# Optimization experiments

Measured on AMD Instinct MI355X. Metric: run time of the kernel, lower is better.

Reference implementation:

```python
import jax, jax.numpy as jnp
import numpy as np

EMBED_DIM = 1024
NUM_HEADS = 16
MICRO_HEADS = 8
HEAD_DIM = EMBED_DIM // NUM_HEADS
N_BLOCKS = NUM_HEADS // MICRO_HEADS
B, N = 2, 2048


def setup_inputs() -> dict:
    key = jax.random.key(0)
    ks = jax.random.split(key, 9)
    s = 1.0 / np.sqrt(EMBED_DIM)
    return {
        "x": jax.random.normal(ks[0], (B, N, EMBED_DIM), dtype=jnp.float32),
        "Wq": jax.random.uniform(ks[1], (EMBED_DIM, EMBED_DIM), jnp.float32, -s, s),
        "bq": jax.random.uniform(ks[2], (EMBED_DIM,), jnp.float32, -s, s),
        "Wk": jax.random.uniform(ks[3], (EMBED_DIM, EMBED_DIM), jnp.float32, -s, s),
        "bk": jax.random.uniform(ks[4], (EMBED_DIM,), jnp.float32, -s, s),
        "Wv": jax.random.uniform(ks[5], (EMBED_DIM, EMBED_DIM), jnp.float32, -s, s),
        "bv": jax.random.uniform(ks[6], (EMBED_DIM,), jnp.float32, -s, s),
        "Wo": jax.random.uniform(ks[7], (EMBED_DIM, EMBED_DIM), jnp.float32, -s, s),
        "bo": jax.random.uniform(ks[8], (EMBED_DIM,), jnp.float32, -s, s),
    }


def _scramble(t, b, n):
    # Replicates torch's Qh[:, :, hs:he, :].contiguous().view(B*mh, N, dh)
    # which is a raw row-major reshape mixing (N, mh) -> (mh, N) per batch.
    # (B, N, E) -> (B, N, nb, mh, dh) -> (B, nb, N, mh, dh) -> raw reshape -> (B, nb, mh, N, dh)
    t = t.reshape(b, n, N_BLOCKS, MICRO_HEADS, HEAD_DIM)
    t = jnp.transpose(t, (0, 2, 1, 3, 4))
    return t.reshape(b, N_BLOCKS, MICRO_HEADS, n, HEAD_DIM)


def reference(x, Wq, bq, Wk, bk, Wv, bv, Wo, bo):
    b, n, e = x.shape
    scale = HEAD_DIM ** -0.5
    Q = x @ Wq.T + bq
    K = x @ Wk.T + bk
    V = x @ Wv.T + bv
    q = _scramble(Q, b, n)  # (B, nb, mh, N, dh)
    k = _scramble(K, b, n)
    v = _scramble(V, b, n)
    s = jnp.einsum("bgmqd,bgmkd->bgmqk", q, k) * scale  # (B, nb, mh, N, N)
    causal = jnp.tril(jnp.ones((n, n), dtype=bool))
    s = jnp.where(causal, s, -jnp.inf)
    p = jax.nn.softmax(s, axis=-1)
    ctx = jnp.einsum("bgmqk,bgmkd->bgmqd", p, v)  # (B, nb, mh, N, dh)
    # inverse raw reshape: (mh, N, dh) -> (N, mh*dh) per (b, g), then concat blocks
    ctx = ctx.reshape(b, N_BLOCKS, n, MICRO_HEADS * HEAD_DIM)
    ctx = jnp.transpose(ctx, (0, 2, 1, 3)).reshape(b, n, e)
    return ctx @ Wo.T + bo
```

## Files before the change

### kernel.cpp

```cpp
#include <hip/hip_runtime.h>
#include <hip/hip_bf16.h>


typedef unsigned short ushortT;
typedef __attribute__((ext_vector_type(8))) short short8;
typedef __attribute__((ext_vector_type(4))) float floatx4;

__device__ inline float bf2f(ushortT u) {
    union { unsigned int i; float f; } v; v.i = ((unsigned int)u) << 16; return v.f;
}
__device__ inline ushortT f2bf(float f) {
    union { float f; unsigned int i; } v; v.f = f;
    unsigned int x = v.i;
    return (ushortT)((x + 0x7fffu + ((x >> 16) & 1u)) >> 16);
}

__device__ inline void gl_lds16(const ushortT* g, ushortT* lds) {
    __builtin_amdgcn_global_load_lds(
        (const __attribute__((address_space(1))) unsigned int*)g,
        (__attribute__((address_space(3))) unsigned int*)lds, 16, 0, 0);
}

__global__ __launch_bounds__(256) void cvt_bf16(
    const float* __restrict__ x,
    const float* __restrict__ Wq, const float* __restrict__ Wk,
    const float* __restrict__ Wv, const float* __restrict__ Wo,
    ushortT* __restrict__ xb, ushortT* __restrict__ Wb)
{
    const unsigned tid = blockIdx.x * 256 + threadIdx.x;
    const size_t e = (size_t)tid * 8;
    const float* src;
    ushortT* dst;
    size_t off;
    if (e < (size_t)(4u << 20)) { src = x; dst = xb; off = e; }
    else {
        const size_t r = e - (size_t)(4u << 20);
        const int wsel = (int)(r >> 20);
        off = r & 0xFFFFFu;
        src = (wsel == 0) ? Wq : (wsel == 1) ? Wk : (wsel == 2) ? Wv : Wo;
        dst = Wb + ((size_t)wsel << 20);
    }
    const float4 f0 = ((const float4*)(src + off))[0];
    const float4 f1 = ((const float4*)(src + off))[1];
    union { __hip_bfloat162 h[4]; uint4 u; } pk;
    pk.h[0] = __float22bfloat162_rn(float2{f0.x, f0.y});
    pk.h[1] = __float22bfloat162_rn(float2{f0.z, f0.w});
    pk.h[2] = __float22bfloat162_rn(float2{f1.x, f1.y});
    pk.h[3] = __float22bfloat162_rn(float2{f1.z, f1.w});
    *(uint4*)(dst + off) = pk.u;
}

template <bool OUT_F32>
__global__ __launch_bounds__(256) void gemm_lds(
    const ushortT* __restrict__ A, const ushortT* __restrict__ Wst,
    const float* __restrict__ b0, const float* __restrict__ b1, const float* __restrict__ b2,
    void* __restrict__ O0, void* __restrict__ O1, void* __restrict__ O2)
{
    __shared__ __align__(16) ushortT As[128 * 64];
    __shared__ __align__(16) ushortT Bs[128 * 64];
    const int t = threadIdx.x;
    const int m0 = blockIdx.y * 128;
    const int n0g = blockIdx.x * 128;
    const int mat = n0g >> 10;
    const int n0 = n0g & 1023;
    const ushortT* W = Wst + ((size_t)mat << 20);
    const float* bias = (mat == 0) ? b0 : (mat == 1) ? b1 : b2;
    void* Out        = (mat == 0) ? O0 : (mat == 1) ? O1 : O2;

    const int w = t >> 6, lane = t & 63;
    const int wm = w >> 1, wn = w & 1;
    const int col16 = lane & 15, quad = lane >> 4;

    floatx4 acc[4][4];
    for (int i = 0; i < 4; i++)
        for (int j = 0; j < 4; j++) acc[i][j] = (floatx4)0.0f;

    const int cid0 = w * 256 + lane;

    for (int k0 = 0; k0 < 1024; k0 += 64) {
        #pragma unroll
        for (int q = 0; q < 4; q++) {
            const int cid = cid0 + q * 64;
            const int row = cid >> 3;
            const int sch = (cid & 7) ^ (row & 7);
            ushortT* dstA = As + (size_t)(w * 256 + q * 64) * 8;
            ushortT* dstB = Bs + (size_t)(w * 256 + q * 64) * 8;
            gl_lds16(A + (size_t)(m0 + row) * 1024 + k0 + sch * 8, dstA);
            gl_lds16(W + (size_t)(n0 + row) * 1024 + k0 + sch * 8, dstB);
        }
        __syncthreads();
        #pragma unroll
        for (int ks = 0; ks < 64; ks += 32) {
            const int cbase = (ks >> 3) + quad;
            const int sw = col16 & 7;
            short8 a[4], b[4];
            #pragma unroll
            for (int i = 0; i < 4; i++) {
                const int row = wm * 64 + i * 16 + col16;
                a[i] = *(const short8*)(As + row * 64 + ((cbase ^ sw) << 3));
            }
            #pragma unroll
            for (int j = 0; j < 4; j++) {
                const int row = wn * 64 + j * 16 + col16;
                b[j] = *(const short8*)(Bs + row * 64 + ((cbase ^ sw) << 3));
            }
            #pragma unroll
            for (int i = 0; i < 4; i++)
                #pragma unroll
                for (int j = 0; j < 4; j++)
                    acc[i][j] = __builtin_amdgcn_mfma_f32_16x16x32_bf16(a[i], b[j], acc[i][j], 0, 0, 0);
        }
        __syncthreads();
    }

    for (int j = 0; j < 4; j++) {
        const int colg = n0 + wn * 64 + j * 16 + col16;
        const float bv = bias[colg];
        for (int i = 0; i < 4; i++) {
            const int rbase = m0 + wm * 64 + i * 16 + quad * 4;
            for (int r = 0; r < 4; r++) {
                const float val = acc[i][j][r] + bv;
                if constexpr (OUT_F32)
                    ((float*)Out)[(size_t)(rbase + r) * 1024 + colg] = val;
                else
                    ((ushortT*)Out)[(size_t)(rbase + r) * 1024 + colg] = f2bf(val);
            }
        }
    }
}

__global__ __launch_bounds__(256) void transpose_v(
    const ushortT* __restrict__ Vb, ushortT* __restrict__ VT)
{
    __shared__ ushortT L[64 * 65];
    const int bid = blockIdx.x;
    const int pt = bid & 31, s = bid >> 5;
    const int bb = s >> 4, g = (s >> 3) & 1, mh = s & 7;
    const size_t baseoff = (size_t)bb * 2048 * 1024 + (size_t)g * 512;
    const int t = threadIdx.x;
    {
        const int pr = t >> 2, seg = t & 3;
        const int i = mh * 2048 + pt * 64 + pr;
        const uint4* src = (const uint4*)(Vb + baseoff + (size_t)(i >> 3) * 1024 + (i & 7) * 64 + seg * 16);
        union { uint4 u[2]; ushortT h[16]; } tmp;
        tmp.u[0] = src[0]; tmp.u[1] = src[1];
        #pragma unroll
        for (int d = 0; d < 16; d++) L[pr * 65 + seg * 16 + d] = tmp.h[d];
    }
    __syncthreads();
    {
        const int dc = t >> 2, pseg = t & 3;
        union { uint4 u[2]; ushortT h[16]; } tmp;
        #pragma unroll
        for (int j = 0; j < 16; j++) tmp.h[j] = L[(pseg * 16 + j) * 65 + dc];
        uint4* dst = (uint4*)(VT + (size_t)s * 64 * 2048 + (size_t)dc * 2048 + pt * 64 + pseg * 16);
        dst[0] = tmp.u[0]; dst[1] = tmp.u[1];
    }
}

__global__ __launch_bounds__(256) void attn(
    const ushortT* __restrict__ Qb, const ushortT* __restrict__ Kb,
    const ushortT* __restrict__ VT, ushortT* __restrict__ Cb)
{
    __shared__ __align__(16) ushortT Qs[128 * 72];
    __shared__ __align__(16) ushortT Ks[2][64 * 64];
    __shared__ __align__(16) ushortT Vs[2][64 * 64];
    __shared__ __align__(16) ushortT Ps[64 * 72];

    const int t = threadIdx.x;
    const int bid = blockIdx.x;
    const int xcd = bid & 7;
    const int jj  = bid >> 3;
    const int s   = xcd * 4 + (jj >> 4);
    const int p   = jj & 15;
    const int qtA = p, qtB = 31 - p;
    const int bb = s >> 4, g = (s >> 3) & 1, mh = s & 7;

    const int w = t >> 6, lane = t & 63;
    const int col16 = lane & 15, quad = lane >> 4;

    const size_t baseoff = (size_t)bb * 2048 * 1024 + (size_t)g * 512;
    const size_t vtbase  = (size_t)s * 64 * 2048;
    const int i0A = mh * 2048 + qtA * 64;
    const int i0B = mh * 2048 + qtB * 64;
    const int qloc = w * 16 + col16;
    const float KL = 0.125f * 1.44269504f;

    {
        const int row = t >> 1, half = t & 1;
        const int i = ((row < 64) ? i0A : i0B) + (row & 63);
        const uint4* src = (const uint4*)(Qb + baseoff + (size_t)(i >> 3) * 1024 + (i & 7) * 64 + half * 32);
        uint4* dst = (uint4*)(Qs + row * 72 + half * 32);
        dst[0] = src[0]; dst[1] = src[1]; dst[2] = src[2]; dst[3] = src[3];
    }

    auto stageKV = [&](int kt, int bsel) {
        ushortT* kd = &Ks[bsel][0] + (size_t)(w * 128) * 8;
        ushortT* vd = &Vs[bsel][0] + (size_t)(w * 128) * 8;
        #pragma unroll
        for (int q = 0; q < 2; q++) {
            const int cid = w * 128 + q * 64 + lane;
            const int row = cid >> 3;
            const int sch = (cid & 7) ^ (row & 7);
            const int jr = mh * 2048 + kt * 64 + row;
            gl_lds16(Kb + baseoff + (size_t)(jr >> 3) * 1024 + (jr & 7) * 64 + sch * 8,
                     kd + q * 64 * 8);
            gl_lds16(VT + vtbase + (size_t)row * 2048 + kt * 64 + sch * 8,
                     vd + q * 64 * 8);
        }
    };

    float m_s[2] = {-1e30f, -1e30f};
    float l_s[2] = {0.f, 0.f};
    floatx4 Oacc[2][4];
    for (int tl = 0; tl < 2; tl++)
        for (int c = 0; c < 4; c++) Oacc[tl][c] = (floatx4)0.0f;

    stageKV(0, 0);
    const int ktmax = qtB;
    for (int kt = 0; kt <= ktmax; ++kt) {
        const int bsel = kt & 1;
        __syncthreads();
        if (kt < ktmax) stageKV(kt + 1, bsel ^ 1);

        #pragma unroll
        for (int tile = 0; tile < 2; ++tile) {
            const int qt = tile ? qtB : qtA;
            if (kt > qt) continue;
            const int qsrow = (tile ? 64 : 0) + qloc;

            floatx4 sc[4];
            for (int c = 0; c < 4; c++) sc[c] = (floatx4)0.0f;
            #pragma unroll
            for (int ks = 0; ks < 64; ks += 32) {
                const short8 bq = *(const short8*)(Qs + qsrow * 72 + ks + quad * 8);
                #pragma unroll
                for (int c = 0; c < 4; c++) {
                    const int krow = c * 16 + col16;
                    const short8 ak = *(const short8*)(&Ks[bsel][0] + krow * 64 +
                                        ((((ks >> 3) + quad) ^ (krow & 7)) << 3));
                    sc[c] = __builtin_amdgcn_mfma_f32_16x16x32_bf16(ak, bq, sc[c], 0, 0, 0);
                }
            }

            const bool diag = (kt == qt);
            float mx = -1e30f;
            #pragma unroll
            for (int c = 0; c < 4; c++)
                #pragma unroll
                for (int r = 0; r < 4; r++) {
                    float v = sc[c][r];
                    if (diag && (c * 16 + quad * 4 + r) > qloc) v = -1e30f;
                    sc[c][r] = v;
                    mx = fmaxf(mx, v);
                }
            mx = fmaxf(mx, __shfl_xor(mx, 16));
            mx = fmaxf(mx, __shfl_xor(mx, 32));
            const float mold = m_s[tile];
            const float mnew = fmaxf(mold, mx);
            const float alpha = exp2f((mold - mnew) * KL);
            m_s[tile] = mnew;
            float sum = 0.f;
            #pragma unroll
            for (int c = 0; c < 4; c++)
                #pragma unroll
                for (int r = 0; r < 4; r++) {
                    const float pv = exp2f((sc[c][r] - mnew) * KL);
                    sc[c][r] = pv;
                    sum += pv;
                }
            sum += __shfl_xor(sum, 16);
            sum += __shfl_xor(sum, 32);
            l_s[tile] = l_s[tile] * alpha + sum;
            #pragma unroll
            for (int c = 0; c < 4; c++) Oacc[tile][c] *= alpha;

            #pragma unroll
            for (int c = 0; c < 4; c++)
                #pragma unroll
                for (int rp = 0; rp < 2; rp++) {
                    union { ushortT h[2]; unsigned int u; } pk;
                    pk.h[0] = f2bf(sc[c][rp * 2]);
                    pk.h[1] = f2bf(sc[c][rp * 2 + 1]);
                    *(unsigned int*)(Ps + qloc * 72 + c * 16 + quad * 4 + rp * 2) = pk.u;
                }

            #pragma unroll
            for (int kk = 0; kk < 64; kk += 32) {
                const short8 bp = *(const short8*)(Ps + qloc * 72 + kk + quad * 8);
                #pragma unroll
                for (int c = 0; c < 4; c++) {
                    const int drow = c * 16 + col16;
                    const short8 av = *(const short8*)(&Vs[bsel][0] + drow * 64 +
                                        ((((kk >> 3) + quad) ^ (drow & 7)) << 3));
                    Oacc[tile][c] = __builtin_amdgcn_mfma_f32_16x16x32_bf16(av, bp, Oacc[tile][c], 0, 0, 0);
                }
            }
        }
    }

    #pragma unroll
    for (int tile = 0; tile < 2; ++tile) {
        const int i = (tile ? i0B : i0A) + qloc;
        const float inv = 1.0f / l_s[tile];
        ushortT* dst = Cb + baseoff + (size_t)(i >> 3) * 1024 + (i & 7) * 64;
        #pragma unroll
        for (int c = 0; c < 4; c++)
            #pragma unroll
            for (int rp = 0; rp < 2; rp++) {
                union { ushortT h[2]; unsigned int u; } pk;
                pk.h[0] = f2bf(Oacc[tile][c][rp * 2] * inv);
                pk.h[1] = f2bf(Oacc[tile][c][rp * 2 + 1] * inv);
                *(unsigned int*)(dst + c * 16 + quad * 4 + rp * 2) = pk.u;
            }
    }
}

extern "C" void kernel_launch(void* const* d_in, const int* in_sizes, int n_in,
                              void* d_out, int out_size, void* d_ws, size_t ws_size,
                              hipStream_t stream)
{
    const float* x  = (const float*)d_in[0];
    const float* Wq = (const float*)d_in[1];
    const float* bq = (const float*)d_in[2];
    const float* Wk = (const float*)d_in[3];
    const float* bk = (const float*)d_in[4];
    const float* Wv = (const float*)d_in[5];
    const float* bv = (const float*)d_in[6];
    const float* Wo = (const float*)d_in[7];
    const float* bo = (const float*)d_in[8];

    const size_t M1 = (size_t)1024 * 1024;
    ushortT* Wb  = (ushortT*)d_ws;
    ushortT* xb  = Wb + 4 * M1;
    ushortT* Qb  = xb + 4 * M1;
    ushortT* Kb  = Qb + 4 * M1;
    ushortT* Vb  = (ushortT*)d_out;
    ushortT* VTb = xb;
    ushortT* Cb  = Qb;

    dim3 blk(256);
    cvt_bf16<<<dim3(4096), blk, 0, stream>>>(x, Wq, Wk, Wv, Wo, xb, Wb);
    gemm_lds<false><<<dim3(24, 32), blk, 0, stream>>>(
        xb, Wb, bq, bk, bv, Qb, Kb, Vb);
    transpose_v<<<dim3(1024), blk, 0, stream>>>(Vb, VTb);
    attn<<<dim3(512), blk, 0, stream>>>(Qb, Kb, VTb, Cb);
    gemm_lds<true><<<dim3(8, 32), blk, 0, stream>>>(
        Cb, Wb + 3 * M1, bo, bo, bo, d_out, d_out, d_out);
}
```

Baseline: 218.7 us.

## Keep Q in registers, swizzle P tile, and use packed bf16 conversions in attention

Result: no change. 216.7 us (-1.0%).

```diff
diff --git a/kernel.cpp b/kernel.cpp
--- a/kernel.cpp
+++ b/kernel.cpp
@@ -162,10 +162,9 @@
     const ushortT* __restrict__ Qb, const ushortT* __restrict__ Kb,
     const ushortT* __restrict__ VT, ushortT* __restrict__ Cb)
 {
-    __shared__ __align__(16) ushortT Qs[128 * 72];
     __shared__ __align__(16) ushortT Ks[2][64 * 64];
     __shared__ __align__(16) ushortT Vs[2][64 * 64];
-    __shared__ __align__(16) ushortT Ps[64 * 72];
+    __shared__ __align__(16) ushortT Ps[64 * 64];
 
     const int t = threadIdx.x;
     const int bid = blockIdx.x;
@@ -184,14 +183,18 @@
     const int i0A = mh * 2048 + qtA * 64;
     const int i0B = mh * 2048 + qtB * 64;
     const int qloc = w * 16 + col16;
+    const int psw = qloc & 7;
     const float KL = 0.125f * 1.44269504f;
 
+    short8 qreg[2][2];
     {
-        const int row = t >> 1, half = t & 1;
-        const int i = ((row < 64) ? i0A : i0B) + (row & 63);
-        const uint4* src = (const uint4*)(Qb + baseoff + (size_t)(i >> 3) * 1024 + (i & 7) * 64 + half * 32);
-        uint4* dst = (uint4*)(Qs + row * 72 + half * 32);
-        dst[0] = src[0]; dst[1] = src[1]; dst[2] = src[2]; dst[3] = src[3];
+        const int iA = i0A + qloc, iB = i0B + qloc;
+        const ushortT* pA = Qb + baseoff + (size_t)(iA >> 3) * 1024 + (iA & 7) * 64;
+        const ushortT* pB = Qb + baseoff + (size_t)(iB >> 3) * 1024 + (iB & 7) * 64;
+        qreg[0][0] = *(const short8*)(pA + quad * 8);
+        qreg[0][1] = *(const short8*)(pA + 32 + quad * 8);
+        qreg[1][0] = *(const short8*)(pB + quad * 8);
+        qreg[1][1] = *(const short8*)(pB + 32 + quad * 8);
     }
 
     auto stageKV = [&](int kt, int bsel) {
@@ -227,13 +230,12 @@
         for (int tile = 0; tile < 2; ++tile) {
             const int qt = tile ? qtB : qtA;
             if (kt > qt) continue;
-            const int qsrow = (tile ? 64 : 0) + qloc;
 
             floatx4 sc[4];
             for (int c = 0; c < 4; c++) sc[c] = (floatx4)0.0f;
             #pragma unroll
-            for (int ks = 0; ks < 64; ks += 32) {
-                const short8 bq = *(const short8*)(Qs + qsrow * 72 + ks + quad * 8);
+            for (int ks = 0; ks < 32 * 2; ks += 32) {
+                const short8 bq = qreg[tile][ks >> 5];
                 #pragma unroll
                 for (int c = 0; c < 4; c++) {
                     const int krow = c * 16 + col16;
@@ -243,29 +245,31 @@
                 }
             }
 
-            const bool diag = (kt == qt);
+            if (kt == qt) {
+                #pragma unroll
+                for (int c = 0; c < 4; c++)
+                    #pragma unroll
+                    for (int r = 0; r < 4; r++)
+                        if ((c * 16 + quad * 4 + r) > qloc) sc[c][r] = -1e30f;
+            }
             float mx = -1e30f;
             #pragma unroll
             for (int c = 0; c < 4; c++)
                 #pragma unroll
-                for (int r = 0; r < 4; r++) {
-                    float v = sc[c][r];
-                    if (diag && (c * 16 + quad * 4 + r) > qloc) v = -1e30f;
-                    sc[c][r] = v;
-                    mx = fmaxf(mx, v);
-                }
+                for (int r = 0; r < 4; r++) mx = fmaxf(mx, sc[c][r]);
             mx = fmaxf(mx, __shfl_xor(mx, 16));
             mx = fmaxf(mx, __shfl_xor(mx, 32));
             const float mold = m_s[tile];
             const float mnew = fmaxf(mold, mx);
             const float alpha = exp2f((mold - mnew) * KL);
             m_s[tile] = mnew;
+            const float mKL = mnew * KL;
             float sum = 0.f;
             #pragma unroll
             for (int c = 0; c < 4; c++)
                 #pragma unroll
                 for (int r = 0; r < 4; r++) {
-                    const float pv = exp2f((sc[c][r] - mnew) * KL);
+                    const float pv = exp2f(__builtin_fmaf(sc[c][r], KL, -mKL));
                     sc[c][r] = pv;
                     sum += pv;
                 }
@@ -276,18 +280,19 @@
             for (int c = 0; c < 4; c++) Oacc[tile][c] *= alpha;
 
             #pragma unroll
-            for (int c = 0; c < 4; c++)
-                #pragma unroll
-                for (int rp = 0; rp < 2; rp++) {
-                    union { ushortT h[2]; unsigned int u; } pk;
-                    pk.h[0] = f2bf(sc[c][rp * 2]);
-                    pk.h[1] = f2bf(sc[c][rp * 2 + 1]);
-                    *(unsigned int*)(Ps + qloc * 72 + c * 16 + quad * 4 + rp * 2) = pk.u;
-                }
-
-            #pragma unroll
-            for (int kk = 0; kk < 64; kk += 32) {
-                const short8 bp = *(const short8*)(Ps + qloc * 72 + kk + quad * 8);
+            for (int c = 0; c < 4; c++) {
+                const int key0 = c * 16 + quad * 4;
+                union { __hip_bfloat162 h[2]; unsigned long long u; } pk2;
+                pk2.h[0] = __float22bfloat162_rn(float2{sc[c][0], sc[c][1]});
+                pk2.h[1] = __float22bfloat162_rn(float2{sc[c][2], sc[c][3]});
+                *(unsigned long long*)(Ps + qloc * 64 +
+                    (((key0 >> 3) ^ psw) << 3) + (key0 & 7)) = pk2.u;
+            }
+
+            #pragma unroll
+            for (int kk = 0; kk < 32 * 2; kk += 32) {
+                const short8 bp = *(const short8*)(Ps + qloc * 64 +
+                                    ((((kk >> 3) + quad) ^ psw) << 3));
                 #pragma unroll
                 for (int c = 0; c < 4; c++) {
                     const int drow = c * 16 + col16;
@@ -305,14 +310,12 @@
         const float inv = 1.0f / l_s[tile];
         ushortT* dst = Cb + baseoff + (size_t)(i >> 3) * 1024 + (i & 7) * 64;
         #pragma unroll
-        for (int c = 0; c < 4; c++)
-            #pragma unroll
-            for (int rp = 0; rp < 2; rp++) {
-                union { ushortT h[2]; unsigned int u; } pk;
-                pk.h[0] = f2bf(Oacc[tile][c][rp * 2] * inv);
-                pk.h[1] = f2bf(Oacc[tile][c][rp * 2 + 1] * inv);
-                *(unsigned int*)(dst + c * 16 + quad * 4 + rp * 2) = pk.u;
-            }
+        for (int c = 0; c < 4; c++) {
+            union { __hip_bfloat162 h[2]; unsigned long long u; } pk2;
+            pk2.h[0] = __float22bfloat162_rn(float2{Oacc[tile][c][0] * inv, Oacc[tile][c][1] * inv});
+            pk2.h[1] = __float22bfloat162_rn(float2{Oacc[tile][c][2] * inv, Oacc[tile][c][3] * inv});
+            *(unsigned long long*)(dst + c * 16 + quad * 4) = pk2.u;
+        }
     }
 }
 
```
